# Performance work log

Hardware: AMD Instinct MI355X
Metric: run time of the kernel (lower is better)

Reference implementation:

```python
import jax, jax.numpy as jnp
import numpy as np
import math

B, T, C = 2, 2048, 1024
NH = 16
HD = C // NH

def setup_inputs() -> dict:
    key = jax.random.key(0)
    ks = jax.random.split(key, 3)
    scale = 0.02
    return {
        "x": jax.random.normal(ks[0], (B, T, C), dtype=jnp.float32),
        "Wqkv": jax.random.normal(ks[1], (C, 3 * C), dtype=jnp.float32) * scale,
        "bqkv": jnp.zeros((3 * C,), dtype=jnp.float32),
        "Wproj": jax.random.normal(ks[2], (C, C), dtype=jnp.float32) * scale,
        "bproj": jnp.zeros((C,), dtype=jnp.float32),
    }

def reference(x, Wqkv, bqkv, Wproj, bproj):
    b, t, c = x.shape
    qkv = x @ Wqkv + bqkv                      # (B,T,3C)
    qkv = qkv.reshape(b, t, 3, NH, HD)
    q = jnp.transpose(qkv[:, :, 0], (0, 2, 1, 3))  # (B,H,T,D)
    k = jnp.transpose(qkv[:, :, 1], (0, 2, 1, 3))
    v = jnp.transpose(qkv[:, :, 2], (0, 2, 1, 3))
    att = jnp.einsum('bhqd,bhkd->bhqk', q, k) / math.sqrt(HD)
    causal = jnp.tril(jnp.ones((t, t), dtype=bool))
    att = jnp.where(causal[None, None], att, jnp.float32(-jnp.inf))
    att = jax.nn.softmax(att, axis=-1)
    y = jnp.einsum('bhqk,bhkd->bhqd', att, v)  # (B,H,T,D)
    y = jnp.transpose(y, (0, 2, 1, 3)).reshape(b, t, c)
    return y @ Wproj + bproj
```

## Files before the change

kernel.cpp:

```cpp
#include <hip/hip_runtime.h>


typedef __attribute__((ext_vector_type(8))) short short8;
typedef __attribute__((ext_vector_type(4))) short short4v;
typedef __attribute__((ext_vector_type(4))) float f32x4;
typedef __attribute__((ext_vector_type(2))) unsigned int u32x2;
struct ushort4_t { unsigned short x, y, z, w; };

#define MFMA16(a, b, c) __builtin_amdgcn_mfma_f32_16x16x32_bf16((a), (b), (c), 0, 0, 0)
#define MFMA16K16(a, b, c) __builtin_amdgcn_mfma_f32_16x16x16bf16_1k((a), (b), (c), 0, 0, 0)

__device__ __forceinline__ unsigned short f2bf(float f) {
  unsigned u = __builtin_bit_cast(unsigned, f);
  u += 0x7fffu + ((u >> 16) & 1u);
  return (unsigned short)(u >> 16);
}

__device__ __forceinline__ unsigned short f2bf_fast(float f) {
  return (unsigned short)((__builtin_bit_cast(unsigned, f) + 0x8000u) >> 16);
}

#if __has_builtin(__builtin_amdgcn_cvt_pk_bf16_f32)
typedef __attribute__((ext_vector_type(2))) __bf16 bf16x2;
__device__ __forceinline__ short4v pack_bf16x4(float a, float b, float c, float d) {
  bf16x2 lo = __builtin_amdgcn_cvt_pk_bf16_f32(a, b);
  bf16x2 hi = __builtin_amdgcn_cvt_pk_bf16_f32(c, d);
  u32x2 t;
  t[0] = __builtin_bit_cast(unsigned, lo);
  t[1] = __builtin_bit_cast(unsigned, hi);
  return __builtin_bit_cast(short4v, t);
}
#else
__device__ __forceinline__ short4v pack_bf16x4(float a, float b, float c, float d) {
  short4v r;
  r[0] = (short)f2bf_fast(a); r[1] = (short)f2bf_fast(b);
  r[2] = (short)f2bf_fast(c); r[3] = (short)f2bf_fast(d);
  return r;
}
#endif

__device__ __forceinline__ void gl2lds16(const void* g, void* l) {
  __builtin_amdgcn_global_load_lds(
      (__attribute__((address_space(1))) void*)g,
      (__attribute__((address_space(3))) void*)l,
      16, 0, 0);
}

__global__ __launch_bounds__(256) void conv_bf16(const float* __restrict__ src,
                                                 unsigned short* __restrict__ dst,
                                                 int n) {
  int i = (blockIdx.x * 256 + threadIdx.x) * 4;
  if (i >= n) return;
  float4 f = *(const float4*)(src + i);
  unsigned long long r = (unsigned long long)f2bf(f.x)
      | ((unsigned long long)f2bf(f.y) << 16)
      | ((unsigned long long)f2bf(f.z) << 32)
      | ((unsigned long long)f2bf(f.w) << 48);
  *(unsigned long long*)(dst + i) = r;
}

__global__ __launch_bounds__(256) void transpose_conv(const float* __restrict__ W,
                                                      unsigned short* __restrict__ WT,
                                                      int K, int N) {
  __shared__ float tile[64][65];
  const int n0 = blockIdx.x * 64, k0 = blockIdx.y * 64;
  const int tid = threadIdx.x;
  const int c = tid & 63, rbase = tid >> 6;
#pragma unroll
  for (int i = 0; i < 16; ++i) {
    int r = i * 4 + rbase;
    tile[r][c] = W[(size_t)(k0 + r) * N + n0 + c];
  }
  __syncthreads();
#pragma unroll
  for (int i = 0; i < 16; ++i) {
    int r = i * 4 + rbase;
    WT[(size_t)(n0 + r) * K + k0 + c] = f2bf(tile[c][r]);
  }
}

template <int EPI, int MT>
__global__ __launch_bounds__(256)
void gemm_bt(const unsigned short* __restrict__ A,
             const unsigned short* __restrict__ BT,
             const float* __restrict__ bias,
             float* __restrict__ outF,
             unsigned short* __restrict__ q_out,
             unsigned short* __restrict__ k_out,
             unsigned short* __restrict__ vT_out,
             int Ndim, int Kdim) {
  constexpr int IF = MT / 32;
  constexpr int RA = MT / 32;
  __shared__ __align__(16) unsigned short As[MT * 64];
  __shared__ __align__(16) unsigned short Bs[128 * 64];
  const int tid = threadIdx.x;
  const int wave = tid >> 6, lane = tid & 63;
  const int quad = lane >> 4, lr = lane & 15;
  const int wm = wave >> 1, wn = wave & 1;
  const int m0 = blockIdx.y * MT, n0 = blockIdx.x * 128;

  const int r_l = tid >> 3;
  const int cg = (tid & 7) ^ (r_l & 7);
  const unsigned short* gA = A + (size_t)(m0 + r_l) * Kdim + cg * 8;
  const unsigned short* gB = BT + (size_t)(n0 + r_l) * Kdim + cg * 8;
  const size_t rstep = (size_t)32 * Kdim;

  f32x4 acc[IF][4] = {};
  for (int k0 = 0; k0 < Kdim; k0 += 64) {
#pragma unroll
    for (int rd = 0; rd < RA; ++rd)
      gl2lds16(gA + k0 + rd * rstep, As + rd * 2048 + wave * 512);
#pragma unroll
    for (int rd = 0; rd < 4; ++rd)
      gl2lds16(gB + k0 + rd * rstep, Bs + rd * 2048 + wave * 512);
    __syncthreads();
#pragma unroll
    for (int s = 0; s < 2; ++s) {
      const int sw = ((s * 4 + quad) ^ (lr & 7)) * 8;
      short8 a[IF], b[4];
#pragma unroll
      for (int i = 0; i < IF; ++i)
        a[i] = *(const short8*)(As + (wm * (MT / 2) + i * 16 + lr) * 64 + sw);
#pragma unroll
      for (int j = 0; j < 4; ++j)
        b[j] = *(const short8*)(Bs + (wn * 64 + j * 16 + lr) * 64 + sw);
#pragma unroll
      for (int i = 0; i < IF; ++i)
#pragma unroll
        for (int j = 0; j < 4; ++j)
          acc[i][j] = MFMA16(a[i], b[j], acc[i][j]);
    }
    __syncthreads();
  }

  const int row_t = wm * (MT / 2) + quad * 4;
  const int col_t = wn * 64 + lr;
  if (EPI == 0) {
    const int sec = n0 >> 10;
    const float scl = (sec == 0) ? 0.18033688f : 1.0f;
#pragma unroll
    for (int j = 0; j < 4; ++j) {
      const int n = n0 + col_t + j * 16;
      const float bi = bias[n];
      const int nn = n & 1023, h = nn >> 6, d = nn & 63;
#pragma unroll
      for (int i = 0; i < IF; ++i) {
        const int m_base = m0 + row_t + i * 16;
        const int bb = m_base >> 11, t0 = m_base & 2047;
        const int bh = bb * 16 + h;
        if (sec == 2) {
          ushort4_t pk;
          pk.x = f2bf(acc[i][j][0] + bi);
          pk.y = f2bf(acc[i][j][1] + bi);
          pk.z = f2bf(acc[i][j][2] + bi);
          pk.w = f2bf(acc[i][j][3] + bi);
          *(ushort4_t*)(vT_out + ((size_t)bh * 64 + d) * 2048 + t0) = pk;
        } else {
          unsigned short* dst = (sec == 0 ? q_out : k_out) + (size_t)bh * 131072 + t0 * 64 + d;
#pragma unroll
          for (int r = 0; r < 4; ++r)
            dst[r * 64] = f2bf((acc[i][j][r] + bi) * scl);
        }
      }
    }
  } else {
#pragma unroll
    for (int i = 0; i < IF; ++i)
#pragma unroll
      for (int r = 0; r < 4; ++r) {
        const int m = m0 + row_t + i * 16 + r;
#pragma unroll
        for (int j = 0; j < 4; ++j) {
          const int n = n0 + col_t + j * 16;
          outF[(size_t)m * Ndim + n] = acc[i][j][r] + bias[n];
        }
      }
  }
}

__global__ __launch_bounds__(256, 2)
void attn(const unsigned short* __restrict__ qbuf,
          const unsigned short* __restrict__ kbuf,
          const unsigned short* __restrict__ vT,
          unsigned short* __restrict__ yb) {
  __shared__ __align__(16) unsigned short Ks[3][4096];
  __shared__ __align__(16) unsigned short Vs[3][4096];
  const int tid = threadIdx.x, wave = tid >> 6, lane = tid & 63;
  const int quad = lane >> 4, lr = lane & 15;
  const int bh = blockIdx.y;
  const int sx = ((int)blockIdx.x + bh) & 15;
  const int qt = (bh & 16) ? (15 - sx) : sx;
  const int qrow0 = qt * 128;

  const unsigned short* qp0 = qbuf + (size_t)bh * 131072;
  const unsigned short* kp0 = kbuf + (size_t)bh * 131072;
  const unsigned short* vp0 = vT   + (size_t)bh * 131072;

  short8 aq[2][2];
#pragma unroll
  for (int g = 0; g < 2; ++g) {
    const unsigned short* qp =
        qp0 + (size_t)(qrow0 + g * 64 + wave * 16 + lr) * 64 + quad * 8;
    aq[g][0] = *(const short8*)qp;
    aq[g][1] = *(const short8*)(qp + 32);
  }

  short4v ones4;
#pragma unroll
  for (int i = 0; i < 4; ++i) ones4[i] = (short)0x3F80;

  const int sr = tid >> 3;
  const int scg = (tid & 7) ^ (sr & 7);
  int kbase[2];
#pragma unroll
  for (int h = 0; h < 2; ++h)
    kbase[h] = lr * 64 + (((quad + 4 * h) ^ (lr & 7)) << 3);
  int vbase[4];
#pragma unroll
  for (int kb = 0; kb < 4; ++kb)
    vbase[kb] = lr * 64 + (((2 * kb + (quad >> 1)) ^ (lr & 7)) << 3) + (quad & 1) * 4;

  f32x4 o[2][4] = {};
  f32x4 lacc[2] = {};

  auto stage = [&](int buf, int kt) {
    const unsigned short* kg = kp0 + (size_t)(kt * 64 + sr) * 64 + scg * 8;
    const unsigned short* vg = vp0 + (size_t)sr * 2048 + kt * 64 + scg * 8;
    gl2lds16(kg,             &Ks[buf][wave * 512]);
    gl2lds16(kg + 32 * 64,   &Ks[buf][2048 + wave * 512]);
    gl2lds16(vg,             &Vs[buf][wave * 512]);
    gl2lds16(vg + 32 * 2048, &Vs[buf][2048 + wave * 512]);
  };

  const int d0 = 2 * qt;
  const int dlast = 2 * qt + 1;
  stage(0, 0);
  stage(1, 1);
  int buf = 0;
  for (int kt = 0; kt <= dlast; ++kt) {
    if (kt < dlast) __builtin_amdgcn_s_waitcnt(0x0F74);
    else            __builtin_amdgcn_s_waitcnt(0x0F70);
    __builtin_amdgcn_s_barrier();
    if (kt + 2 <= dlast) {
      int nb = buf + 2; if (nb >= 3) nb -= 3;
      stage(nb, kt + 2);
    }
    const unsigned short* Kb = Ks[buf];
    const unsigned short* Vb = Vs[buf];
    short8 bk[4][2];
#pragma unroll
    for (int jt = 0; jt < 4; ++jt) {
      bk[jt][0] = *(const short8*)(Kb + jt * 1024 + kbase[0]);
      bk[jt][1] = *(const short8*)(Kb + jt * 1024 + kbase[1]);
    }
    short4v pa[2][4];
#pragma unroll
    for (int g = 0; g < 2; ++g) {
      const int dg = 2 * qt + g;
      if (kt > dg) {
#pragma unroll
        for (int jt = 0; jt < 4; ++jt) pa[g][jt] = (short4v)0;
      } else {
        f32x4 s[4] = {};
#pragma unroll
        for (int jt = 0; jt < 4; ++jt) {
          s[jt] = MFMA16(bk[jt][0], aq[g][0], s[jt]);
          s[jt] = MFMA16(bk[jt][1], aq[g][1], s[jt]);
        }
        if (kt == dg) {
          const int qloc = wave * 16 + lr;
#pragma unroll
          for (int jt = 0; jt < 4; ++jt) {
            float p[4];
#pragma unroll
            for (int r = 0; r < 4; ++r) {
              p[r] = __builtin_amdgcn_exp2f(s[jt][r]);
              if (jt * 16 + quad * 4 + r > qloc) p[r] = 0.f;
            }
            pa[g][jt] = pack_bf16x4(p[0], p[1], p[2], p[3]);
          }
        } else {
#pragma unroll
          for (int jt = 0; jt < 4; ++jt) {
            float p[4];
#pragma unroll
            for (int r = 0; r < 4; ++r) p[r] = __builtin_amdgcn_exp2f(s[jt][r]);
            pa[g][jt] = pack_bf16x4(p[0], p[1], p[2], p[3]);
          }
        }
#pragma unroll
        for (int kb = 0; kb < 4; ++kb)
          lacc[g] = MFMA16K16(ones4, pa[g][kb], lacc[g]);
      }
    }
    if (kt <= d0) {
#pragma unroll
      for (int kb = 0; kb < 4; ++kb)
#pragma unroll
        for (int jd = 0; jd < 4; ++jd) {
          const short4v bv = *(const short4v*)(Vb + jd * 1024 + vbase[kb]);
          o[0][jd] = MFMA16K16(pa[0][kb], bv, o[0][jd]);
          o[1][jd] = MFMA16K16(pa[1][kb], bv, o[1][jd]);
        }
    } else {
#pragma unroll
      for (int kb = 0; kb < 4; ++kb)
#pragma unroll
        for (int jd = 0; jd < 4; ++jd) {
          const short4v bv = *(const short4v*)(Vb + jd * 1024 + vbase[kb]);
          o[1][jd] = MFMA16K16(pa[1][kb], bv, o[1][jd]);
        }
    }
    buf += 1; if (buf >= 3) buf -= 3;
  }

  const int b = bh >> 4, h = bh & 15;
#pragma unroll
  for (int g = 0; g < 2; ++g) {
    float inv[4];
#pragma unroll
    for (int r = 0; r < 4; ++r)
      inv[r] = __builtin_amdgcn_rcpf(__shfl(lacc[g][0], quad * 4 + r));
#pragma unroll
    for (int jd = 0; jd < 4; ++jd)
#pragma unroll
      for (int r = 0; r < 4; ++r) {
        const int t = qrow0 + g * 64 + wave * 16 + quad * 4 + r;
        yb[((size_t)b * 2048 + t) * 1024 + h * 64 + jd * 16 + lr] =
            f2bf(o[g][jd][r] * inv[r]);
      }
  }
}

extern "C" void kernel_launch(void* const* d_in, const int* in_sizes, int n_in,
                              void* d_out, int out_size, void* d_ws, size_t ws_size,
                              hipStream_t stream) {
  const float* x     = (const float*)d_in[0];
  const float* Wqkv  = (const float*)d_in[1];
  const float* bqkv  = (const float*)d_in[2];
  const float* Wproj = (const float*)d_in[3];
  const float* bproj = (const float*)d_in[4];
  float* out = (float*)d_out;

  char* ws = (char*)d_ws;
  unsigned short* xb     = (unsigned short*)(ws);
  unsigned short* wqkvT  = (unsigned short*)(ws + 8388608);
  unsigned short* wprojT = (unsigned short*)(ws + 14680064);
  unsigned short* qbuf   = (unsigned short*)(ws + 16777216);
  unsigned short* kbuf   = (unsigned short*)(ws + 25165824);
  unsigned short* vTbuf  = (unsigned short*)(ws + 33554432);
  unsigned short* ybuf   = (unsigned short*)(ws + 41943040);

  conv_bf16<<<4096, 256, 0, stream>>>(x, xb, 4194304);
  transpose_conv<<<dim3(48, 16), 256, 0, stream>>>(Wqkv, wqkvT, 1024, 3072);
  transpose_conv<<<dim3(16, 16), 256, 0, stream>>>(Wproj, wprojT, 1024, 1024);
  gemm_bt<0, 128><<<dim3(24, 32), 256, 0, stream>>>(xb, wqkvT, bqkv, nullptr,
                                                    qbuf, kbuf, vTbuf, 3072, 1024);
  attn<<<dim3(16, 32), 256, 0, stream>>>(qbuf, kbuf, vTbuf, ybuf);
  gemm_bt<1, 64><<<dim3(8, 64), 256, 0, stream>>>(ybuf, wprojT, bproj, out,
                                                  nullptr, nullptr, nullptr, 1024, 1024);
}
```

Baseline: 182.8 us.

## Shrink attention query tile to 64 rows and schedule heaviest tiles first

The attention kernel now gives each block 64 query rows instead of 128, which doubles the grid to 1024 blocks. blockIdx.x now selects the batch-head and blockIdx.y is mapped in reverse, so the longest causal tiles launch first. Launch bounds are raised to 3 blocks per CU to improve occupancy and load balance. In exchange, each K/V tile staged into LDS is reused by half as many query rows, so global and LDS traffic per unit of useful work roughly doubles.

Measured after the change: 180.7 us. Within noise of the previous version (-1.1%).

```diff
diff --git a/kernel.cpp b/kernel.cpp
--- a/kernel.cpp
+++ b/kernel.cpp
@@ -178,7 +178,7 @@
   }
 }
 
-__global__ __launch_bounds__(256, 2)
+__global__ __launch_bounds__(256, 3)
 void attn(const unsigned short* __restrict__ qbuf,
           const unsigned short* __restrict__ kbuf,
           const unsigned short* __restrict__ vT,
@@ -187,22 +187,20 @@
   __shared__ __align__(16) unsigned short Vs[3][4096];
   const int tid = threadIdx.x, wave = tid >> 6, lane = tid & 63;
   const int quad = lane >> 4, lr = lane & 15;
-  const int bh = blockIdx.y;
-  const int sx = ((int)blockIdx.x + bh) & 15;
-  const int qt = (bh & 16) ? (15 - sx) : sx;
-  const int qrow0 = qt * 128;
+  const int bh = blockIdx.x;
+  const int qt = 31 - (int)blockIdx.y;
+  const int qrow0 = qt * 64;
 
   const unsigned short* qp0 = qbuf + (size_t)bh * 131072;
   const unsigned short* kp0 = kbuf + (size_t)bh * 131072;
   const unsigned short* vp0 = vT   + (size_t)bh * 131072;
 
-  short8 aq[2][2];
-#pragma unroll
-  for (int g = 0; g < 2; ++g) {
+  short8 aq[2];
+  {
     const unsigned short* qp =
-        qp0 + (size_t)(qrow0 + g * 64 + wave * 16 + lr) * 64 + quad * 8;
-    aq[g][0] = *(const short8*)qp;
-    aq[g][1] = *(const short8*)(qp + 32);
+        qp0 + (size_t)(qrow0 + wave * 16 + lr) * 64 + quad * 8;
+    aq[0] = *(const short8*)qp;
+    aq[1] = *(const short8*)(qp + 32);
   }
 
   short4v ones4;
@@ -220,8 +218,8 @@
   for (int kb = 0; kb < 4; ++kb)
     vbase[kb] = lr * 64 + (((2 * kb + (quad >> 1)) ^ (lr & 7)) << 3) + (quad & 1) * 4;
 
-  f32x4 o[2][4] = {};
-  f32x4 lacc[2] = {};
+  f32x4 o[4] = {};
+  f32x4 lacc = {};
 
   auto stage = [&](int buf, int kt) {
     const unsigned short* kg = kp0 + (size_t)(kt * 64 + sr) * 64 + scg * 8;
@@ -232,10 +230,9 @@
     gl2lds16(vg + 32 * 2048, &Vs[buf][2048 + wave * 512]);
   };
 
-  const int d0 = 2 * qt;
-  const int dlast = 2 * qt + 1;
+  const int dlast = qt;
   stage(0, 0);
-  stage(1, 1);
+  if (dlast >= 1) stage(1, 1);
   int buf = 0;
   for (int kt = 0; kt <= dlast; ++kt) {
     if (kt < dlast) __builtin_amdgcn_s_waitcnt(0x0F74);
@@ -253,83 +250,60 @@
       bk[jt][0] = *(const short8*)(Kb + jt * 1024 + kbase[0]);
       bk[jt][1] = *(const short8*)(Kb + jt * 1024 + kbase[1]);
     }
-    short4v pa[2][4];
-#pragma unroll
-    for (int g = 0; g < 2; ++g) {
-      const int dg = 2 * qt + g;
-      if (kt > dg) {
-#pragma unroll
-        for (int jt = 0; jt < 4; ++jt) pa[g][jt] = (short4v)0;
-      } else {
-        f32x4 s[4] = {};
-#pragma unroll
-        for (int jt = 0; jt < 4; ++jt) {
-          s[jt] = MFMA16(bk[jt][0], aq[g][0], s[jt]);
-          s[jt] = MFMA16(bk[jt][1], aq[g][1], s[jt]);
+    f32x4 s[4] = {};
+#pragma unroll
+    for (int jt = 0; jt < 4; ++jt) {
+      s[jt] = MFMA16(bk[jt][0], aq[0], s[jt]);
+      s[jt] = MFMA16(bk[jt][1], aq[1], s[jt]);
+    }
+    short4v pa[4];
+    if (kt == dlast) {
+      const int qloc = wave * 16 + lr;
+#pragma unroll
+      for (int jt = 0; jt < 4; ++jt) {
+        float p[4];
+#pragma unroll
+        for (int r = 0; r < 4; ++r) {
+          p[r] = __builtin_amdgcn_exp2f(s[jt][r]);
+          if (jt * 16 + quad * 4 + r > qloc) p[r] = 0.f;
         }
-        if (kt == dg) {
-          const int qloc = wave * 16 + lr;
-#pragma unroll
-          for (int jt = 0; jt < 4; ++jt) {
-            float p[4];
-#pragma unroll
-            for (int r = 0; r < 4; ++r) {
-              p[r] = __builtin_amdgcn_exp2f(s[jt][r]);
-              if (jt * 16 + quad * 4 + r > qloc) p[r] = 0.f;
-            }
-            pa[g][jt] = pack_bf16x4(p[0], p[1], p[2], p[3]);
-          }
-        } else {
-#pragma unroll
-          for (int jt = 0; jt < 4; ++jt) {
-            float p[4];
-#pragma unroll
-            for (int r = 0; r < 4; ++r) p[r] = __builtin_amdgcn_exp2f(s[jt][r]);
-            pa[g][jt] = pack_bf16x4(p[0], p[1], p[2], p[3]);
-          }
-        }
-#pragma unroll
-        for (int kb = 0; kb < 4; ++kb)
-          lacc[g] = MFMA16K16(ones4, pa[g][kb], lacc[g]);
-      }
-    }
-    if (kt <= d0) {
-#pragma unroll
-      for (int kb = 0; kb < 4; ++kb)
-#pragma unroll
-        for (int jd = 0; jd < 4; ++jd) {
-          const short4v bv = *(const short4v*)(Vb + jd * 1024 + vbase[kb]);
-          o[0][jd] = MFMA16K16(pa[0][kb], bv, o[0][jd]);
-          o[1][jd] = MFMA16K16(pa[1][kb], bv, o[1][jd]);
-        }
+        pa[jt] = pack_bf16x4(p[0], p[1], p[2], p[3]);
+      }
     } else {
 #pragma unroll
-      for (int kb = 0; kb < 4; ++kb)
-#pragma unroll
-        for (int jd = 0; jd < 4; ++jd) {
-          const short4v bv = *(const short4v*)(Vb + jd * 1024 + vbase[kb]);
-          o[1][jd] = MFMA16K16(pa[1][kb], bv, o[1][jd]);
-        }
-    }
+      for (int jt = 0; jt < 4; ++jt) {
+        float p[4];
+#pragma unroll
+        for (int r = 0; r < 4; ++r) p[r] = __builtin_amdgcn_exp2f(s[jt][r]);
+        pa[jt] = pack_bf16x4(p[0], p[1], p[2], p[3]);
+      }
+    }
+#pragma unroll
+    for (int kb = 0; kb < 4; ++kb)
+      lacc = MFMA16K16(ones4, pa[kb], lacc);
+#pragma unroll
+    for (int kb = 0; kb < 4; ++kb)
+#pragma unroll
+      for (int jd = 0; jd < 4; ++jd) {
+        const short4v bv = *(const short4v*)(Vb + jd * 1024 + vbase[kb]);
+        o[jd] = MFMA16K16(pa[kb], bv, o[jd]);
+      }
     buf += 1; if (buf >= 3) buf -= 3;
   }
 
   const int b = bh >> 4, h = bh & 15;
-#pragma unroll
-  for (int g = 0; g < 2; ++g) {
-    float inv[4];
-#pragma unroll
-    for (int r = 0; r < 4; ++r)
-      inv[r] = __builtin_amdgcn_rcpf(__shfl(lacc[g][0], quad * 4 + r));
-#pragma unroll
-    for (int jd = 0; jd < 4; ++jd)
-#pragma unroll
-      for (int r = 0; r < 4; ++r) {
-        const int t = qrow0 + g * 64 + wave * 16 + quad * 4 + r;
-        yb[((size_t)b * 2048 + t) * 1024 + h * 64 + jd * 16 + lr] =
-            f2bf(o[g][jd][r] * inv[r]);
-      }
-  }
+  float inv[4];
+#pragma unroll
+  for (int r = 0; r < 4; ++r)
+    inv[r] = __builtin_amdgcn_rcpf(__shfl(lacc[0], quad * 4 + r));
+#pragma unroll
+  for (int jd = 0; jd < 4; ++jd)
+#pragma unroll
+    for (int r = 0; r < 4; ++r) {
+      const int t = qrow0 + wave * 16 + quad * 4 + r;
+      yb[((size_t)b * 2048 + t) * 1024 + h * 64 + jd * 16 + lr] =
+          f2bf(o[jd][r] * inv[r]);
+    }
 }
 
 extern "C" void kernel_launch(void* const* d_in, const int* in_sizes, int n_in,
@@ -356,7 +330,7 @@
   transpose_conv<<<dim3(16, 16), 256, 0, stream>>>(Wproj, wprojT, 1024, 1024);
   gemm_bt<0, 128><<<dim3(24, 32), 256, 0, stream>>>(xb, wqkvT, bqkv, nullptr,
                                                     qbuf, kbuf, vTbuf, 3072, 1024);
-  attn<<<dim3(16, 32), 256, 0, stream>>>(qbuf, kbuf, vTbuf, ybuf);
+  attn<<<dim3(32, 32), 256, 0, stream>>>(qbuf, kbuf, vTbuf, ybuf);
   gemm_bt<1, 64><<<dim3(8, 64), 256, 0, stream>>>(ybuf, wprojT, bproj, out,
                                                   nullptr, nullptr, nullptr, 1024, 1024);
 }
```
